# Optimization experiments

Hardware: AMD Instinct MI355X
Metric: run time of the kernel (lower is better)

## Reference

```python
import jax, jax.numpy as jnp
import numpy as np

TAU = 2.0  # self.temperature
EPS = 1e-7


def setup_inputs() -> dict:
    key = jax.random.key(0)
    kx, km, kw, kb, kc, kg = jax.random.split(key, 6)
    B, S, H = 8, 2048, 512
    G, V, D = 2, 320, 256  # num_groups, num_vars, codevector_dim
    hidden_states = jax.random.normal(kx, (B, S, H), dtype=jnp.float32)
    mask_time_indices = jax.random.randint(km, (B, S), 0, 2) > 0
    # nn.Linear(H, G*V)
    lim = 1.0 / np.sqrt(H)
    W_proj = jax.random.uniform(kw, (H, G * V), minval=-lim, maxval=lim, dtype=jnp.float32)
    b_proj = jax.random.uniform(kb, (G * V,), minval=-lim, maxval=lim, dtype=jnp.float32)
    codevectors = jax.random.normal(kc, (1, G * V, D // G), dtype=jnp.float32)
    # precomputed gumbel noise for determinism (torch samples inside gumbel_softmax)
    gumbels = jax.random.gumbel(kg, (B * S * G, V), dtype=jnp.float32)
    return {
        "hidden_states": hidden_states,
        "mask_time_indices": mask_time_indices,
        "W_proj": W_proj,
        "b_proj": b_proj,
        "codevectors": codevectors,
        "gumbels": gumbels,
    }


def reference(hidden_states, mask_time_indices, W_proj, b_proj, codevectors, gumbels):
    B, S, H = hidden_states.shape
    GV = W_proj.shape[1]
    V = gumbels.shape[-1]
    G = GV // V
    N = B * S

    logits = hidden_states @ W_proj + b_proj              # [B,S,G*V]
    flat = logits.reshape(N * G, V).astype(jnp.float32)    # [N*G, V]

    # gumbel_softmax(tau=TAU, hard=True) with straight-through estimator
    y_soft = jax.nn.softmax((flat + gumbels) / TAU, axis=-1)
    y_hard = jax.nn.one_hot(jnp.argmax(y_soft, axis=-1), V, dtype=y_soft.dtype)
    probs = y_hard + y_soft - jax.lax.stop_gradient(y_soft)  # [N*G, V]

    # perplexity from the (non-gumbel) soft distribution, masked marginals
    soft_dist = jax.nn.softmax(flat.reshape(N, G, V), axis=-1)
    m = mask_time_indices.reshape(-1).astype(soft_dist.dtype)  # [N]
    marginal = jnp.einsum('ngv,n->gv', soft_dist, m) / jnp.sum(m)
    perplexity = jnp.exp(-jnp.sum(marginal * jnp.log(marginal + EPS), axis=-1)).sum()

    # codebook combine: grouped one-hot mixture (avoids [N, G*V, D/G] blowup)
    cb = codevectors.reshape(G, V, -1)                     # [G, V, D/G]
    codevecs = jnp.einsum('ngv,gvd->ngd', probs.reshape(N, G, V), cb)
    codevecs = codevecs.reshape(B, S, -1)                  # [B, S, D]
    return codevecs, perplexity
```

## Files before the change

### kernel.cpp

```cpp
#include <hip/hip_runtime.h>
#include <hip/hip_bf16.h>
#include <math.h>

constexpr int Mn = 16384;
constexpr int Kd = 512;
constexpr int GV = 640;
constexpr int Vn = 320;
constexpr int Gn = 2;
constexpr int DG = 128;
constexpr float EPSc = 1e-7f;

constexpr int K2 = 1536;
constexpr int KA = 1024;
constexpr int NT = K2 / 32;

typedef _Float16 half8 __attribute__((ext_vector_type(8)));
typedef _Float16 half4 __attribute__((ext_vector_type(4)));
typedef float floatx4 __attribute__((ext_vector_type(4)));

__global__ __launch_bounds__(256) void convert_all(const float* __restrict__ h,
                                                   const float* __restrict__ W,
                                                   _Float16* __restrict__ A2,
                                                   _Float16* __restrict__ B2T) {
  const int bid = blockIdx.x;
  if (bid < 2048) {
    const int total = Mn * Kd / 4;
    for (int idx = bid * 256 + threadIdx.x; idx < total; idx += 2048 * 256) {
      float4 x = reinterpret_cast<const float4*>(h)[idx];
      int m = idx >> 7;
      int c = (idx & 127) << 2;
      half4 h0, h1;
      float xs[4] = {x.x, x.y, x.z, x.w};
#pragma unroll
      for (int j = 0; j < 4; ++j) {
        _Float16 a = (_Float16)xs[j];
        h0[j] = a;
        h1[j] = (_Float16)(xs[j] - (float)a);
      }
      *reinterpret_cast<half4*>(&A2[(size_t)m * KA + c]) = h0;
      *reinterpret_cast<half4*>(&A2[(size_t)m * KA + Kd + c]) = h1;
    }
  } else {
    const int b2 = bid - 2048;
    const int wave = threadIdx.x >> 6, lane = threadIdx.x & 63;
    const int n = b2 * 4 + wave;
    _Float16* row = B2T + (size_t)n * K2;
#pragma unroll
    for (int j = 0; j < 8; ++j) {
      const int k = lane + 64 * j;
      const float w = W[(size_t)k * GV + n];
      const _Float16 w0 = (_Float16)w;
      const _Float16 w1 = (_Float16)(w - (float)w0);
      row[k] = w0;
      row[Kd + k] = w0;
      row[2 * Kd + k] = w1;
    }
  }
}

__global__ __launch_bounds__(256, 5) void gemm_f16x2(const _Float16* __restrict__ A2,
                                                     const _Float16* __restrict__ B2T,
                                                     const float* __restrict__ bias,
                                                     float* __restrict__ C) {
  __shared__ _Float16 As[2][128 * 32];
  __shared__ _Float16 Bs[2][64 * 32];

  const int bid = blockIdx.x;
  const int sw = (bid & 7) * 160 + (bid >> 3);
  const int mt = sw / 10, nt = sw % 10;
  const int m0 = mt * 128, n0 = nt * 64;

  const int t = threadIdx.x, wv = t >> 6, l = t & 63;
  const int wr = wv >> 1, wc = wv & 1;
  const int lr = l & 15, lk = l >> 4;

  floatx4 acc[4][2] = {};

  auto stage = [&](int buf, int kt) {
    const int k2 = kt * 32;
    const int kA = k2 >= KA ? k2 - KA : k2;
#pragma unroll
    for (int i = 0; i < 2; ++i) {
      const int idx = i * 256 + t;
      const int r = idx >> 2, s2 = idx & 3;
      const int sp = s2 ^ ((r >> 1) & 3);
      const _Float16* ga = A2 + (size_t)(m0 + r) * KA + kA + sp * 8;
      _Float16* la = &As[buf][(i * 256 + wv * 64) * 8];
      __builtin_amdgcn_global_load_lds((const __attribute__((address_space(1))) void*)ga,
                                       (__attribute__((address_space(3))) void*)la, 16, 0, 0);
    }
    {
      const int idx = t;
      const int r = idx >> 2, s2 = idx & 3;
      const int sp = s2 ^ ((r >> 1) & 3);
      const _Float16* gb = B2T + (size_t)(n0 + r) * K2 + k2 + sp * 8;
      _Float16* lb = &Bs[buf][(wv * 64) * 8];
      __builtin_amdgcn_global_load_lds((const __attribute__((address_space(1))) void*)gb,
                                       (__attribute__((address_space(3))) void*)lb, 16, 0, 0);
    }
  };

  stage(0, 0);
  __syncthreads();
  int cur = 0;
  for (int kt = 0; kt < NT; ++kt) {
    if (kt + 1 < NT) stage(cur ^ 1, kt + 1);

    half8 af[4], bf[2];
#pragma unroll
    for (int mi = 0; mi < 4; ++mi) {
      const int row = wr * 64 + mi * 16 + lr;
      const int sp = lk ^ ((row >> 1) & 3);
      af[mi] = *reinterpret_cast<const half8*>(&As[cur][row * 32 + sp * 8]);
    }
#pragma unroll
    for (int ni = 0; ni < 2; ++ni) {
      const int row = wc * 32 + ni * 16 + lr;
      const int sp = lk ^ ((row >> 1) & 3);
      bf[ni] = *reinterpret_cast<const half8*>(&Bs[cur][row * 32 + sp * 8]);
    }
#pragma unroll
    for (int mi = 0; mi < 4; ++mi)
#pragma unroll
      for (int ni = 0; ni < 2; ++ni)
        acc[mi][ni] = __builtin_amdgcn_mfma_f32_16x16x32_f16(af[mi], bf[ni], acc[mi][ni], 0, 0, 0);

    __syncthreads();
    cur ^= 1;
  }

#pragma unroll
  for (int ni = 0; ni < 2; ++ni) {
    const int gcol = n0 + wc * 32 + ni * 16 + lr;
    const float bv = bias[gcol];
#pragma unroll
    for (int mi = 0; mi < 4; ++mi) {
      const int grow = m0 + wr * 64 + mi * 16 + lk * 4;
#pragma unroll
      for (int j = 0; j < 4; ++j)
        C[(size_t)(grow + j) * GV + gcol] = acc[mi][ni][j] + bv;
    }
  }
}

__global__ __launch_bounds__(256) void row_kernel(const float* __restrict__ logits,
                                                  const float* __restrict__ gumbels,
                                                  const int* __restrict__ mask,
                                                  const float* __restrict__ codevectors,
                                                  float* __restrict__ out,
                                                  float* __restrict__ part,
                                                  float* __restrict__ marg) {
  __shared__ float lmarg[GV];
  const int wave = threadIdx.x >> 6, lane = threadIdx.x & 63;
  const int g = wave & 1;
  const int stream = wave >> 1;
  const int nbase = blockIdx.x * 16 + stream * 8;

  if (threadIdx.x < 16) {
    const int mk = (mask[blockIdx.x * 16 + threadIdx.x] != 0) ? 1 : 0;
    const unsigned long long b = __ballot(mk);
    if (threadIdx.x == 0) atomicAdd(&marg[GV], (float)__popcll(b & 0xFFFFull));
  }

  float acc[5] = {0.f, 0.f, 0.f, 0.f, 0.f};

  for (int it = 0; it < 4; ++it) {
    const int na = nbase + it * 2, nb = na + 1;
    const float* lrA = logits + (size_t)na * GV + g * Vn;
    const float* grA = gumbels + ((size_t)na * Gn + g) * Vn;
    const float* lrB = logits + (size_t)nb * GV + g * Vn;
    const float* grB = gumbels + ((size_t)nb * Gn + g) * Vn;

    float4 lA = reinterpret_cast<const float4*>(lrA)[lane];
    float4 gA = reinterpret_cast<const float4*>(grA)[lane];
    float lsA = lrA[256 + lane], gsA = grA[256 + lane];
    float4 lB = reinterpret_cast<const float4*>(lrB)[lane];
    float4 gB = reinterpret_cast<const float4*>(grB)[lane];
    float lsB = lrB[256 + lane], gsB = grB[256 + lane];

    float vA[5] = {lA.x, lA.y, lA.z, lA.w, lsA};
    float yA[5] = {lA.x + gA.x, lA.y + gA.y, lA.z + gA.z, lA.w + gA.w, lsA + gsA};
    float vB[5] = {lB.x, lB.y, lB.z, lB.w, lsB};
    float yB[5] = {lB.x + gB.x, lB.y + gB.y, lB.z + gB.z, lB.w + gB.w, lsB + gsB};

    float amA = yA[0], amB = yB[0];
    int aiA = lane * 4, aiB = lane * 4;
#pragma unroll
    for (int j = 1; j < 5; ++j) {
      const int v = (j < 4) ? lane * 4 + j : 256 + lane;
      if (yA[j] > amA) { amA = yA[j]; aiA = v; }
      if (yB[j] > amB) { amB = yB[j]; aiB = v; }
    }
#pragma unroll
    for (int off = 32; off; off >>= 1) {
      const float oA = __shfl_xor(amA, off);
      const int iA = __shfl_xor(aiA, off);
      if (oA > amA || (oA == amA && iA < aiA)) { amA = oA; aiA = iA; }
      const float oB = __shfl_xor(amB, off);
      const int iB = __shfl_xor(aiB, off);
      if (oB > amB || (oB == amB && iB < aiB)) { amB = oB; aiB = iB; }
    }

    float eA[5], eB[5], sA = 0.f, sB = 0.f;
#pragma unroll
    for (int j = 0; j < 5; ++j) {
      eA[j] = expf(vA[j]); sA += eA[j];
      eB[j] = expf(vB[j]); sB += eB[j];
    }
#pragma unroll
    for (int off = 32; off; off >>= 1) {
      sA += __shfl_xor(sA, off);
      sB += __shfl_xor(sB, off);
    }
    const float invA = 1.0f / sA, invB = 1.0f / sB;

    if (mask[na] != 0) {
#pragma unroll
      for (int j = 0; j < 5; ++j) acc[j] += eA[j] * invA;
    }
    if (mask[nb] != 0) {
#pragma unroll
      for (int j = 0; j < 5; ++j) acc[j] += eB[j] * invB;
    }

    const float* cvA = codevectors + ((size_t)g * Vn + aiA) * DG;
    float* orA = out + (size_t)na * (Gn * DG) + g * DG;
    orA[lane] = cvA[lane];
    orA[lane + 64] = cvA[lane + 64];
    const float* cvB = codevectors + ((size_t)g * Vn + aiB) * DG;
    float* orB = out + (size_t)nb * (Gn * DG) + g * DG;
    orB[lane] = cvB[lane];
    orB[lane + 64] = cvB[lane + 64];
  }

  if (stream == 0) {
#pragma unroll
    for (int j = 0; j < 4; ++j) lmarg[g * Vn + lane * 4 + j] = acc[j];
    lmarg[g * Vn + 256 + lane] = acc[4];
  }
  __syncthreads();
  if (stream == 1) {
#pragma unroll
    for (int j = 0; j < 4; ++j) lmarg[g * Vn + lane * 4 + j] += acc[j];
    lmarg[g * Vn + 256 + lane] += acc[4];
  }
  __syncthreads();
  float* prow = part + (size_t)blockIdx.x * GV;
  for (int i = threadIdx.x; i < GV; i += 256) prow[i] = lmarg[i];
}

__global__ __launch_bounds__(64) void reduce_marg(const float* __restrict__ part,
                                                  float* __restrict__ marg) {
  const int c = blockIdx.x * 64 + threadIdx.x;
  const int r0 = blockIdx.y * 64;
  float s = 0.f;
#pragma unroll 8
  for (int r = 0; r < 64; ++r) s += part[(size_t)(r0 + r) * GV + c];
  atomicAdd(&marg[c], s);
}

__global__ __launch_bounds__(640) void finalize(const float* __restrict__ marg,
                                                float* __restrict__ out_pp) {
  __shared__ float wred[10];
  const int t = threadIdx.x, wave = t >> 6, lane = t & 63;
  const float msum = marg[GV];

  const float p = marg[t] / msum;
  float e = p * logf(p + EPSc);
#pragma unroll
  for (int off = 32; off; off >>= 1) e += __shfl_xor(e, off);
  if (lane == 0) wred[wave] = e;
  __syncthreads();
  if (t == 0) {
    const float e0 = wred[0] + wred[1] + wred[2] + wred[3] + wred[4];
    const float e1 = wred[5] + wred[6] + wred[7] + wred[8] + wred[9];
    out_pp[0] = expf(-e0) + expf(-e1);
  }
}

extern "C" void kernel_launch(void* const* d_in, const int* in_sizes, int n_in,
                              void* d_out, int out_size, void* d_ws, size_t ws_size,
                              hipStream_t stream) {
  const float* hidden      = (const float*)d_in[0];
  const int*   mask        = (const int*)d_in[1];
  const float* W           = (const float*)d_in[2];
  const float* bias        = (const float*)d_in[3];
  const float* codevectors = (const float*)d_in[4];
  const float* gumbels     = (const float*)d_in[5];
  float* out = (float*)d_out;

  const size_t logitsBytes = (size_t)Mn * GV * sizeof(float);
  const size_t a2Off       = logitsBytes + 8192;
  const size_t a2Bytes     = (size_t)Mn * KA * sizeof(_Float16);
  const size_t b2tOff      = a2Off + a2Bytes;

  float*    logits = (float*)d_ws;
  float*    marg   = (float*)((char*)d_ws + logitsBytes);
  _Float16* A2     = (_Float16*)((char*)d_ws + a2Off);
  _Float16* B2T    = (_Float16*)((char*)d_ws + b2tOff);
  float*    part   = (float*)A2;

  hipMemsetAsync(marg, 0, (GV + 1) * sizeof(float), stream);

  convert_all<<<2208, 256, 0, stream>>>(hidden, W, A2, B2T);
  gemm_f16x2<<<1280, 256, 0, stream>>>(A2, B2T, bias, logits);
  row_kernel<<<Mn / 16, 256, 0, stream>>>(logits, gumbels, mask, codevectors, out, part, marg);
  reduce_marg<<<dim3(10, 16), 64, 0, stream>>>(part, marg);
  finalize<<<1, 640, 0, stream>>>(marg, out + (size_t)Mn * (Gn * DG));
}
```

Before: 117.7 us.

## Split GEMM K across two halves with 128x128 tiles, sum partials in row kernel

```diff
diff --git a/kernel.cpp b/kernel.cpp
--- a/kernel.cpp
+++ b/kernel.cpp
@@ -13,6 +13,7 @@
 constexpr int K2 = 1536;
 constexpr int KA = 1024;
 constexpr int NT = K2 / 32;
+constexpr int NTH = 24;
 
 typedef _Float16 half8 __attribute__((ext_vector_type(8)));
 typedef _Float16 half4 __attribute__((ext_vector_type(4)));
@@ -58,26 +59,30 @@
   }
 }
 
-__global__ __launch_bounds__(256, 5) void gemm_f16x2(const _Float16* __restrict__ A2,
-                                                     const _Float16* __restrict__ B2T,
-                                                     const float* __restrict__ bias,
-                                                     float* __restrict__ C) {
+__global__ __launch_bounds__(256, 5) void gemm_splitk(const _Float16* __restrict__ A2,
+                                                      const _Float16* __restrict__ B2T,
+                                                      const float* __restrict__ bias,
+                                                      float* __restrict__ C0,
+                                                      float* __restrict__ C1) {
   __shared__ _Float16 As[2][128 * 32];
-  __shared__ _Float16 Bs[2][64 * 32];
+  __shared__ _Float16 Bs[2][128 * 32];
 
   const int bid = blockIdx.x;
   const int sw = (bid & 7) * 160 + (bid >> 3);
-  const int mt = sw / 10, nt = sw % 10;
-  const int m0 = mt * 128, n0 = nt * 64;
+  const int kh = sw / 640;
+  const int tile = sw - kh * 640;
+  const int mt = tile / 5, nt = tile % 5;
+  const int m0 = mt * 128, n0 = nt * 128;
+  const int kbase = kh * NTH;
 
   const int t = threadIdx.x, wv = t >> 6, l = t & 63;
   const int wr = wv >> 1, wc = wv & 1;
   const int lr = l & 15, lk = l >> 4;
 
-  floatx4 acc[4][2] = {};
-
-  auto stage = [&](int buf, int kt) {
-    const int k2 = kt * 32;
+  floatx4 acc[4][4] = {};
+
+  auto stage = [&](int buf, int ktg) {
+    const int k2 = ktg * 32;
     const int kA = k2 >= KA ? k2 - KA : k2;
 #pragma unroll
     for (int i = 0; i < 2; ++i) {
@@ -89,6 +94,89 @@
       __builtin_amdgcn_global_load_lds((const __attribute__((address_space(1))) void*)ga,
                                        (__attribute__((address_space(3))) void*)la, 16, 0, 0);
     }
+#pragma unroll
+    for (int i = 0; i < 2; ++i) {
+      const int idx = i * 256 + t;
+      const int r = idx >> 2, s2 = idx & 3;
+      const int sp = s2 ^ ((r >> 1) & 3);
+      const _Float16* gb = B2T + (size_t)(n0 + r) * K2 + k2 + sp * 8;
+      _Float16* lb = &Bs[buf][(i * 256 + wv * 64) * 8];
+      __builtin_amdgcn_global_load_lds((const __attribute__((address_space(1))) void*)gb,
+                                       (__attribute__((address_space(3))) void*)lb, 16, 0, 0);
+    }
+  };
+
+  stage(0, kbase);
+  __syncthreads();
+  int cur = 0;
+  for (int kt = 0; kt < NTH; ++kt) {
+    if (kt + 1 < NTH) stage(cur ^ 1, kbase + kt + 1);
+
+    half8 af[4], bf[4];
+#pragma unroll
+    for (int mi = 0; mi < 4; ++mi) {
+      const int row = wr * 64 + mi * 16 + lr;
+      const int sp = lk ^ ((row >> 1) & 3);
+      af[mi] = *reinterpret_cast<const half8*>(&As[cur][row * 32 + sp * 8]);
+    }
+#pragma unroll
+    for (int ni = 0; ni < 4; ++ni) {
+      const int row = wc * 64 + ni * 16 + lr;
+      const int sp = lk ^ ((row >> 1) & 3);
+      bf[ni] = *reinterpret_cast<const half8*>(&Bs[cur][row * 32 + sp * 8]);
+    }
+#pragma unroll
+    for (int mi = 0; mi < 4; ++mi)
+#pragma unroll
+      for (int ni = 0; ni < 4; ++ni)
+        acc[mi][ni] = __builtin_amdgcn_mfma_f32_16x16x32_f16(af[mi], bf[ni], acc[mi][ni], 0, 0, 0);
+
+    __syncthreads();
+    cur ^= 1;
+  }
+
+  float* C = kh ? C1 : C0;
+#pragma unroll
+  for (int ni = 0; ni < 4; ++ni) {
+    const int gcol = n0 + wc * 64 + ni * 16 + lr;
+    const float bv = kh ? 0.f : bias[gcol];
+#pragma unroll
+    for (int mi = 0; mi < 4; ++mi) {
+      const int grow = m0 + wr * 64 + mi * 16 + lk * 4;
+#pragma unroll
+      for (int j = 0; j < 4; ++j)
+        C[(size_t)(grow + j) * GV + gcol] = acc[mi][ni][j] + bv;
+    }
+  }
+}
+
+__global__ __launch_bounds__(256, 5) void gemm_f16x2(const _Float16* __restrict__ A2,
+                                                     const _Float16* __restrict__ B2T,
+                                                     const float* __restrict__ bias,
+                                                     float* __restrict__ C) {
+  __shared__ _Float16 As[2][128 * 32];
+  __shared__ _Float16 Bs[2][64 * 32];
+  const int bid = blockIdx.x;
+  const int sw = (bid & 7) * 160 + (bid >> 3);
+  const int mt = sw / 10, nt = sw % 10;
+  const int m0 = mt * 128, n0 = nt * 64;
+  const int t = threadIdx.x, wv = t >> 6, l = t & 63;
+  const int wr = wv >> 1, wc = wv & 1;
+  const int lr = l & 15, lk = l >> 4;
+  floatx4 acc[4][2] = {};
+  auto stage = [&](int buf, int kt) {
+    const int k2 = kt * 32;
+    const int kA = k2 >= KA ? k2 - KA : k2;
+#pragma unroll
+    for (int i = 0; i < 2; ++i) {
+      const int idx = i * 256 + t;
+      const int r = idx >> 2, s2 = idx & 3;
+      const int sp = s2 ^ ((r >> 1) & 3);
+      const _Float16* ga = A2 + (size_t)(m0 + r) * KA + kA + sp * 8;
+      _Float16* la = &As[buf][(i * 256 + wv * 64) * 8];
+      __builtin_amdgcn_global_load_lds((const __attribute__((address_space(1))) void*)ga,
+                                       (__attribute__((address_space(3))) void*)la, 16, 0, 0);
+    }
     {
       const int idx = t;
       const int r = idx >> 2, s2 = idx & 3;
@@ -99,13 +187,11 @@
                                        (__attribute__((address_space(3))) void*)lb, 16, 0, 0);
     }
   };
-
   stage(0, 0);
   __syncthreads();
   int cur = 0;
   for (int kt = 0; kt < NT; ++kt) {
     if (kt + 1 < NT) stage(cur ^ 1, kt + 1);
-
     half8 af[4], bf[2];
 #pragma unroll
     for (int mi = 0; mi < 4; ++mi) {
@@ -124,11 +210,9 @@
 #pragma unroll
       for (int ni = 0; ni < 2; ++ni)
         acc[mi][ni] = __builtin_amdgcn_mfma_f32_16x16x32_f16(af[mi], bf[ni], acc[mi][ni], 0, 0, 0);
-
     __syncthreads();
     cur ^= 1;
   }
-
 #pragma unroll
   for (int ni = 0; ni < 2; ++ni) {
     const int gcol = n0 + wc * 32 + ni * 16 + lr;
@@ -143,7 +227,9 @@
   }
 }
 
-__global__ __launch_bounds__(256) void row_kernel(const float* __restrict__ logits,
+__global__ __launch_bounds__(256) void row_kernel(const float* __restrict__ l0,
+                                                  const float* __restrict__ l1,
+                                                  const int two,
                                                   const float* __restrict__ gumbels,
                                                   const int* __restrict__ mask,
                                                   const float* __restrict__ codevectors,
@@ -166,17 +252,27 @@
 
   for (int it = 0; it < 4; ++it) {
     const int na = nbase + it * 2, nb = na + 1;
-    const float* lrA = logits + (size_t)na * GV + g * Vn;
+    const size_t offA = (size_t)na * GV + g * Vn;
+    const size_t offB = (size_t)nb * GV + g * Vn;
     const float* grA = gumbels + ((size_t)na * Gn + g) * Vn;
-    const float* lrB = logits + (size_t)nb * GV + g * Vn;
     const float* grB = gumbels + ((size_t)nb * Gn + g) * Vn;
 
-    float4 lA = reinterpret_cast<const float4*>(lrA)[lane];
+    float4 lA = reinterpret_cast<const float4*>(l0 + offA)[lane];
+    float lsA = (l0 + offA)[256 + lane];
+    float4 lB = reinterpret_cast<const float4*>(l0 + offB)[lane];
+    float lsB = (l0 + offB)[256 + lane];
+    if (two) {
+      float4 mA = reinterpret_cast<const float4*>(l1 + offA)[lane];
+      lA.x += mA.x; lA.y += mA.y; lA.z += mA.z; lA.w += mA.w;
+      lsA += (l1 + offA)[256 + lane];
+      float4 mB = reinterpret_cast<const float4*>(l1 + offB)[lane];
+      lB.x += mB.x; lB.y += mB.y; lB.z += mB.z; lB.w += mB.w;
+      lsB += (l1 + offB)[256 + lane];
+    }
     float4 gA = reinterpret_cast<const float4*>(grA)[lane];
-    float lsA = lrA[256 + lane], gsA = grA[256 + lane];
-    float4 lB = reinterpret_cast<const float4*>(lrB)[lane];
+    float gsA = grA[256 + lane];
     float4 gB = reinterpret_cast<const float4*>(grB)[lane];
-    float lsB = lrB[256 + lane], gsB = grB[256 + lane];
+    float gsB = grB[256 + lane];
 
     float vA[5] = {lA.x, lA.y, lA.z, lA.w, lsA};
     float yA[5] = {lA.x + gA.x, lA.y + gA.y, lA.z + gA.z, lA.w + gA.w, lsA + gsA};
@@ -289,22 +385,42 @@
   const float* gumbels     = (const float*)d_in[5];
   float* out = (float*)d_out;
 
-  const size_t logitsBytes = (size_t)Mn * GV * sizeof(float);
-  const size_t a2Off       = logitsBytes + 8192;
-  const size_t a2Bytes     = (size_t)Mn * KA * sizeof(_Float16);
-  const size_t b2tOff      = a2Off + a2Bytes;
-
-  float*    logits = (float*)d_ws;
-  float*    marg   = (float*)((char*)d_ws + logitsBytes);
-  _Float16* A2     = (_Float16*)((char*)d_ws + a2Off);
-  _Float16* B2T    = (_Float16*)((char*)d_ws + b2tOff);
-  float*    part   = (float*)A2;
-
-  hipMemsetAsync(marg, 0, (GV + 1) * sizeof(float), stream);
-
-  convert_all<<<2208, 256, 0, stream>>>(hidden, W, A2, B2T);
-  gemm_f16x2<<<1280, 256, 0, stream>>>(A2, B2T, bias, logits);
-  row_kernel<<<Mn / 16, 256, 0, stream>>>(logits, gumbels, mask, codevectors, out, part, marg);
-  reduce_marg<<<dim3(10, 16), 64, 0, stream>>>(part, marg);
-  finalize<<<1, 640, 0, stream>>>(marg, out + (size_t)Mn * (Gn * DG));
-}
+  const size_t cBytes   = (size_t)Mn * GV * sizeof(float);
+  const size_t c1Off    = cBytes;
+  const size_t margOff  = 2 * cBytes;
+  const size_t a2Off    = margOff + 8192;
+  const size_t a2Bytes  = (size_t)Mn * KA * sizeof(_Float16);
+  const size_t b2tOff   = a2Off + a2Bytes;
+  const size_t b2tBytes = (size_t)GV * K2 * sizeof(_Float16);
+  const size_t needBig  = b2tOff + b2tBytes;
+
+  if (ws_size >= needBig) {
+    float*    C0   = (float*)d_ws;
+    float*    C1   = (float*)((char*)d_ws + c1Off);
+    float*    marg = (float*)((char*)d_ws + margOff);
+    _Float16* A2   = (_Float16*)((char*)d_ws + a2Off);
+    _Float16* B2T  = (_Float16*)((char*)d_ws + b2tOff);
+    float*    part = (float*)A2;
+
+    hipMemsetAsync(marg, 0, (GV + 1) * sizeof(float), stream);
+    convert_all<<<2208, 256, 0, stream>>>(hidden, W, A2, B2T);
+    gemm_splitk<<<1280, 256, 0, stream>>>(A2, B2T, bias, C0, C1);
+    row_kernel<<<Mn / 16, 256, 0, stream>>>(C0, C1, 1, gumbels, mask, codevectors, out, part, marg);
+    reduce_marg<<<dim3(10, 16), 64, 0, stream>>>(part, marg);
+    finalize<<<1, 640, 0, stream>>>(marg, out + (size_t)Mn * (Gn * DG));
+  } else {
+    const size_t fa2Off  = cBytes + 8192;
+    float*    C0   = (float*)d_ws;
+    float*    marg = (float*)((char*)d_ws + cBytes);
+    _Float16* A2   = (_Float16*)((char*)d_ws + fa2Off);
+    _Float16* B2T  = (_Float16*)((char*)d_ws + fa2Off + a2Bytes);
+    float*    part = (float*)A2;
+
+    hipMemsetAsync(marg, 0, (GV + 1) * sizeof(float), stream);
+    convert_all<<<2208, 256, 0, stream>>>(hidden, W, A2, B2T);
+    gemm_f16x2<<<1280, 256, 0, stream>>>(A2, B2T, bias, C0);
+    row_kernel<<<Mn / 16, 256, 0, stream>>>(C0, C0, 0, gumbels, mask, codevectors, out, part, marg);
+    reduce_marg<<<dim3(10, 16), 64, 0, stream>>>(part, marg);
+    finalize<<<1, 640, 0, stream>>>(marg, out + (size_t)Mn * (Gn * DG));
+  }
+}
```

Result: slower. 130.9 us (+11.2%).

## Widen GEMM tile to 128x128 with 4-stage LDS pipeline and vmcnt waits

Applied to the files above, without the earlier changes.

```diff
diff --git a/kernel.cpp b/kernel.cpp
--- a/kernel.cpp
+++ b/kernel.cpp
@@ -17,6 +17,8 @@
 typedef _Float16 half8 __attribute__((ext_vector_type(8)));
 typedef _Float16 half4 __attribute__((ext_vector_type(4)));
 typedef float floatx4 __attribute__((ext_vector_type(4)));
+
+#define WAITV(N) asm volatile("s_waitcnt vmcnt(" #N ")" ::: "memory")
 
 __global__ __launch_bounds__(256) void convert_all(const float* __restrict__ h,
                                                    const float* __restrict__ W,
@@ -58,80 +60,106 @@
   }
 }
 
-__global__ __launch_bounds__(256, 5) void gemm_f16x2(const _Float16* __restrict__ A2,
+__global__ __launch_bounds__(256, 2) void gemm_f16x2(const _Float16* __restrict__ A2,
                                                      const _Float16* __restrict__ B2T,
                                                      const float* __restrict__ bias,
                                                      float* __restrict__ C) {
-  __shared__ _Float16 As[2][128 * 32];
-  __shared__ _Float16 Bs[2][64 * 32];
+  __shared__ _Float16 As[4 * 128 * 32];
+  __shared__ _Float16 Bs[4 * 128 * 32];
 
   const int bid = blockIdx.x;
-  const int sw = (bid & 7) * 160 + (bid >> 3);
-  const int mt = sw / 10, nt = sw % 10;
-  const int m0 = mt * 128, n0 = nt * 64;
+  const int sw = (bid & 7) * 80 + (bid >> 3);
+  const int mt = sw / 5, nt = sw % 5;
+  const int m0 = mt * 128, n0 = nt * 128;
 
   const int t = threadIdx.x, wv = t >> 6, l = t & 63;
   const int wr = wv >> 1, wc = wv & 1;
   const int lr = l & 15, lk = l >> 4;
 
-  floatx4 acc[4][2] = {};
-
-  auto stage = [&](int buf, int kt) {
-    const int k2 = kt * 32;
+  floatx4 acc[4][4] = {};
+
+  auto stage = [&](int buf, int ktg) {
+    const int k2 = ktg * 32;
     const int kA = k2 >= KA ? k2 - KA : k2;
+    _Float16* abase = &As[buf * 4096];
+    _Float16* bbase = &Bs[buf * 4096];
 #pragma unroll
     for (int i = 0; i < 2; ++i) {
       const int idx = i * 256 + t;
       const int r = idx >> 2, s2 = idx & 3;
       const int sp = s2 ^ ((r >> 1) & 3);
       const _Float16* ga = A2 + (size_t)(m0 + r) * KA + kA + sp * 8;
-      _Float16* la = &As[buf][(i * 256 + wv * 64) * 8];
+      _Float16* la = abase + (i * 256 + wv * 64) * 8;
       __builtin_amdgcn_global_load_lds((const __attribute__((address_space(1))) void*)ga,
                                        (__attribute__((address_space(3))) void*)la, 16, 0, 0);
     }
-    {
-      const int idx = t;
+#pragma unroll
+    for (int i = 0; i < 2; ++i) {
+      const int idx = i * 256 + t;
       const int r = idx >> 2, s2 = idx & 3;
       const int sp = s2 ^ ((r >> 1) & 3);
       const _Float16* gb = B2T + (size_t)(n0 + r) * K2 + k2 + sp * 8;
-      _Float16* lb = &Bs[buf][(wv * 64) * 8];
+      _Float16* lb = bbase + (i * 256 + wv * 64) * 8;
       __builtin_amdgcn_global_load_lds((const __attribute__((address_space(1))) void*)gb,
                                        (__attribute__((address_space(3))) void*)lb, 16, 0, 0);
     }
   };
 
-  stage(0, 0);
-  __syncthreads();
-  int cur = 0;
-  for (int kt = 0; kt < NT; ++kt) {
-    if (kt + 1 < NT) stage(cur ^ 1, kt + 1);
-
-    half8 af[4], bf[2];
+  auto compute = [&](int buf) {
+    const _Float16* abase = &As[buf * 4096];
+    const _Float16* bbase = &Bs[buf * 4096];
+    half8 af[4], bf[4];
 #pragma unroll
     for (int mi = 0; mi < 4; ++mi) {
       const int row = wr * 64 + mi * 16 + lr;
       const int sp = lk ^ ((row >> 1) & 3);
-      af[mi] = *reinterpret_cast<const half8*>(&As[cur][row * 32 + sp * 8]);
-    }
-#pragma unroll
-    for (int ni = 0; ni < 2; ++ni) {
-      const int row = wc * 32 + ni * 16 + lr;
+      af[mi] = *reinterpret_cast<const half8*>(&abase[row * 32 + sp * 8]);
+    }
+#pragma unroll
+    for (int ni = 0; ni < 4; ++ni) {
+      const int row = wc * 64 + ni * 16 + lr;
       const int sp = lk ^ ((row >> 1) & 3);
-      bf[ni] = *reinterpret_cast<const half8*>(&Bs[cur][row * 32 + sp * 8]);
+      bf[ni] = *reinterpret_cast<const half8*>(&bbase[row * 32 + sp * 8]);
     }
 #pragma unroll
     for (int mi = 0; mi < 4; ++mi)
 #pragma unroll
-      for (int ni = 0; ni < 2; ++ni)
+      for (int ni = 0; ni < 4; ++ni)
         acc[mi][ni] = __builtin_amdgcn_mfma_f32_16x16x32_f16(af[mi], bf[ni], acc[mi][ni], 0, 0, 0);
-
-    __syncthreads();
-    cur ^= 1;
-  }
-
-#pragma unroll
-  for (int ni = 0; ni < 2; ++ni) {
-    const int gcol = n0 + wc * 32 + ni * 16 + lr;
+  };
+
+  stage(0, 0);
+  stage(1, 1);
+  stage(2, 2);
+
+#pragma unroll 1
+  for (int kt = 0; kt < NT - 3; ++kt) {
+    WAITV(8);
+    __builtin_amdgcn_s_barrier();
+    __builtin_amdgcn_sched_barrier(0);
+    compute(kt & 3);
+    __builtin_amdgcn_s_barrier();
+    __builtin_amdgcn_sched_barrier(0);
+    stage((kt + 3) & 3, kt + 3);
+  }
+  WAITV(8);
+  __builtin_amdgcn_s_barrier();
+  __builtin_amdgcn_sched_barrier(0);
+  compute((NT - 3) & 3);
+  __builtin_amdgcn_s_barrier();
+  WAITV(4);
+  __builtin_amdgcn_s_barrier();
+  __builtin_amdgcn_sched_barrier(0);
+  compute((NT - 2) & 3);
+  __builtin_amdgcn_s_barrier();
+  WAITV(0);
+  __builtin_amdgcn_s_barrier();
+  __builtin_amdgcn_sched_barrier(0);
+  compute((NT - 1) & 3);
+
+#pragma unroll
+  for (int ni = 0; ni < 4; ++ni) {
+    const int gcol = n0 + wc * 64 + ni * 16 + lr;
     const float bv = bias[gcol];
 #pragma unroll
     for (int mi = 0; mi < 4; ++mi) {
@@ -289,21 +317,20 @@
   const float* gumbels     = (const float*)d_in[5];
   float* out = (float*)d_out;
 
-  const size_t logitsBytes = (size_t)Mn * GV * sizeof(float);
-  const size_t a2Off       = logitsBytes + 8192;
-  const size_t a2Bytes     = (size_t)Mn * KA * sizeof(_Float16);
-  const size_t b2tOff      = a2Off + a2Bytes;
+  const size_t cBytes  = (size_t)Mn * GV * sizeof(float);
+  const size_t a2Off   = cBytes + 8192;
+  const size_t a2Bytes = (size_t)Mn * KA * sizeof(_Float16);
+  const size_t b2tOff  = a2Off + a2Bytes;
 
   float*    logits = (float*)d_ws;
-  float*    marg   = (float*)((char*)d_ws + logitsBytes);
+  float*    marg   = (float*)((char*)d_ws + cBytes);
   _Float16* A2     = (_Float16*)((char*)d_ws + a2Off);
   _Float16* B2T    = (_Float16*)((char*)d_ws + b2tOff);
   float*    part   = (float*)A2;
 
   hipMemsetAsync(marg, 0, (GV + 1) * sizeof(float), stream);
-
   convert_all<<<2208, 256, 0, stream>>>(hidden, W, A2, B2T);
-  gemm_f16x2<<<1280, 256, 0, stream>>>(A2, B2T, bias, logits);
+  gemm_f16x2<<<640, 256, 0, stream>>>(A2, B2T, bias, logits);
   row_kernel<<<Mn / 16, 256, 0, stream>>>(logits, gumbels, mask, codevectors, out, part, marg);
   reduce_marg<<<dim3(10, 16), 64, 0, stream>>>(part, marg);
   finalize<<<1, 640, 0, stream>>>(marg, out + (size_t)Mn * (Gn * DG));
```

Result: slower. 122.1 us (+3.7%).
